# Optimization experiments

Measured on AMD Instinct MI355X. Metric: run time of the kernel, lower is better.

## Reference

```python
import jax, jax.numpy as jnp
import numpy as np

FILL_VAL = -1
B, S, H, L = 16, 512, 768, 25


def _lstm_dir(x, w_ih, w_hh, b_ih, b_hh, reverse=False):
    # x: [B,T,I]; PyTorch gate order i,f,g,o
    if reverse:
        x = x[:, ::-1]
    xg = jnp.einsum('bti,gi->btg', x, w_ih) + b_ih + b_hh  # [B,T,4H]
    nh = w_hh.shape[1]

    def step(carry, xt):
        h, c = carry
        g = xt + h @ w_hh.T
        i, f, gg, o = jnp.split(g, 4, axis=-1)
        c = jax.nn.sigmoid(f) * c + jax.nn.sigmoid(i) * jnp.tanh(gg)
        h = jax.nn.sigmoid(o) * jnp.tanh(c)
        return (h, c), h

    z = jnp.zeros((x.shape[0], nh), x.dtype)
    _, hs = jax.lax.scan(step, (z, z), jnp.swapaxes(xg, 0, 1))
    hs = jnp.swapaxes(hs, 0, 1)  # [B,T,H]
    return hs[:, ::-1] if reverse else hs


def _crf_nll(emissions, tags, mask, trans, start, end):
    # torchcrf-style NLL, reduction='token_mean'. emissions [B,T,L], tags [B,T], mask bool [B,T]
    maskf = mask.astype(emissions.dtype)
    emit = jnp.take_along_axis(emissions, tags[..., None], axis=-1)[..., 0]  # [B,T]
    trans_sc = trans[tags[:, :-1], tags[:, 1:]]  # [B,T-1]
    num = start[tags[:, 0]] + emit[:, 0] + jnp.sum((trans_sc + emit[:, 1:]) * maskf[:, 1:], axis=1)
    lengths = mask.sum(axis=1)
    last_tags = tags[jnp.arange(tags.shape[0]), lengths - 1]
    num = num + end[last_tags]

    em_t = jnp.swapaxes(emissions, 0, 1)  # [T,B,L]
    mk_t = jnp.swapaxes(mask, 0, 1)

    def step(alpha, inp):
        e_t, m_t = inp
        nxt = jax.nn.logsumexp(alpha[:, :, None] + trans[None] + e_t[:, None, :], axis=1)
        return jnp.where(m_t[:, None], nxt, alpha), None

    alpha0 = start[None] + em_t[0]
    alpha, _ = jax.lax.scan(step, alpha0, (em_t[1:], mk_t[1:]))
    denom = jax.nn.logsumexp(alpha + end[None], axis=1)
    llh = num - denom
    return -(llh.sum() / maskf.sum())


def setup_inputs() -> dict:
    key = jax.random.key(0)
    ks = jax.random.split(key, 32)

    def u(k, shape, s):
        return jax.random.uniform(k, shape, jnp.float32, -s, s)

    s = 1.0 / float(np.sqrt(H))
    hidden = jax.random.normal(ks[0], (B, S, H), jnp.float32)
    labels = jax.random.randint(ks[1], (B, S), 0, L)
    lengths = jax.random.randint(ks[2], (B,), S // 2, S + 1)
    targets = jnp.where(jnp.arange(S)[None, :] < lengths[:, None], labels, FILL_VAL).astype(jnp.int32)

    inp = {'hidden': hidden, 'targets': targets}
    # 2-layer bidirectional LSTM params; layer 1 input is 2H
    names = [('l0', H), ('l0r', H), ('l1', 2 * H), ('l1r', 2 * H)]
    ki = 3
    for nm, insz in names:
        inp['w_ih_' + nm] = u(ks[ki], (4 * H, insz), s); ki += 1
        inp['w_hh_' + nm] = u(ks[ki], (4 * H, H), s); ki += 1
        inp['b_ih_' + nm] = u(ks[ki], (4 * H,), s); ki += 1
        inp['b_hh_' + nm] = u(ks[ki], (4 * H,), s); ki += 1
    inp['clf_w'] = u(ks[ki], (L, 2 * H), 1.0 / float(np.sqrt(2 * H))); ki += 1
    inp['clf_b'] = u(ks[ki], (L,), 1.0 / float(np.sqrt(2 * H))); ki += 1
    inp['crf_trans'] = u(ks[ki], (L, L), 0.1); ki += 1
    inp['crf_start'] = u(ks[ki], (L,), 0.1); ki += 1
    inp['crf_end'] = u(ks[ki], (L,), 0.1)
    return inp


def reference(hidden, targets,
              w_ih_l0, w_hh_l0, b_ih_l0, b_hh_l0,
              w_ih_l0r, w_hh_l0r, b_ih_l0r, b_hh_l0r,
              w_ih_l1, w_hh_l1, b_ih_l1, b_hh_l1,
              w_ih_l1r, w_hh_l1r, b_ih_l1r, b_hh_l1r,
              clf_w, clf_b, crf_trans, crf_start, crf_end):
    mask = targets != FILL_VAL
    tags = jnp.where(mask, targets, 0)
    h1 = jnp.concatenate([
        _lstm_dir(hidden, w_ih_l0, w_hh_l0, b_ih_l0, b_hh_l0),
        _lstm_dir(hidden, w_ih_l0r, w_hh_l0r, b_ih_l0r, b_hh_l0r, reverse=True)], axis=-1)
    h2 = jnp.concatenate([
        _lstm_dir(h1, w_ih_l1, w_hh_l1, b_ih_l1, b_hh_l1),
        _lstm_dir(h1, w_ih_l1r, w_hh_l1r, b_ih_l1r, b_hh_l1r, reverse=True)], axis=-1)
    logits = jnp.tanh(h2) @ clf_w.T + clf_b  # [B,S,L]
    return _crf_nll(logits, tags, mask, crf_trans, crf_start, crf_end)
```

## Files before the change

kernel.cpp:

```cpp
#include <hip/hip_runtime.h>
#include <cstdint>
#include <cstddef>

#define B   16
#define SEQ 512
#define HD  768
#define G4  3072
#define NL  25
#define NBLK 96

using u16 = unsigned short;
using u32 = uint32_t;
using u64 = unsigned long long;

#define XGD ((size_t)96*SEQ*512)

__device__ __forceinline__ float bf2f(u16 u){
  union { float f; u32 i; } v; v.i = ((u32)u) << 16; return v.f;
}
__device__ __forceinline__ u16 f2bf(float f){
  union { float f; u32 i; } v; v.f = f;
  u32 r = v.i + 0x7FFFu + ((v.i >> 16) & 1u);
  return (u16)(r >> 16);
}
__device__ __forceinline__ float asf(u32 u){ union { float f; u32 i; } v; v.i = u; return v.f; }
__device__ __forceinline__ float sigm(float x){ return 1.f/(1.f + __expf(-x)); }
__device__ __forceinline__ float tanhfast(float x){ return 1.f - 2.f/(__expf(2.f*x) + 1.f); }

typedef __attribute__((ext_vector_type(8))) short bf16x8;
typedef __attribute__((ext_vector_type(4))) float f32x4;

__device__ __forceinline__ void stage_to_lds(u16* dst, const u16* src){
  *(uint4*)dst = *(const uint4*)src;
}
__device__ __forceinline__ void stage_to_lds(u16* dst, const float* src){
  float4 a = *(const float4*)src;
  float4 b = *(const float4*)(src + 4);
  uint4 v;
  v.x = (u32)f2bf(a.x) | ((u32)f2bf(a.y) << 16);
  v.y = (u32)f2bf(a.z) | ((u32)f2bf(a.w) << 16);
  v.z = (u32)f2bf(b.x) | ((u32)f2bf(b.y) << 16);
  v.w = (u32)f2bf(b.z) | ((u32)f2bf(b.w) << 16);
  *(uint4*)dst = v;
}

struct BPtrs { const float* bi[4]; const float* bh[4]; };

__global__ void prep_bias(BPtrs p, float* __restrict__ bias){
  int idx = blockIdx.x*blockDim.x + threadIdx.x;
  if (idx < 4*G4){
    int lid = idx / G4, g = idx % G4;
    bias[idx] = p.bi[lid][g] + p.bh[lid][g];
  }
}

template<typename AT>
__global__ __launch_bounds__(256) void gemm_xg_mfma(const AT* __restrict__ A, int K,
    const float* __restrict__ W, const float* __restrict__ bias, u16* __restrict__ out)
{
  __shared__ u16 As[128][72];
  __shared__ u16 Bs[128][72];
  const int tid = threadIdx.x;
  const int bm = blockIdx.y * 128;
  const int bn = blockIdx.x * 128;
  const int wid = tid >> 6, lane = tid & 63;
  const int wr = wid >> 1, wc = wid & 1;
  const int kq = lane >> 4, rl = lane & 15;

  f32x4 acc[4][4];
  #pragma unroll
  for (int mf = 0; mf < 4; mf++)
    #pragma unroll
    for (int nf = 0; nf < 4; nf++) acc[mf][nf] = (f32x4){0.f,0.f,0.f,0.f};

  for (int k0 = 0; k0 < K; k0 += 64){
    #pragma unroll
    for (int u = 0; u < 4; u++){
      int c = tid + u*256;
      int r = c >> 3, q = c & 7;
      stage_to_lds(&As[r][q*8], A + (size_t)(bm + r)*K + k0 + q*8);
      stage_to_lds(&Bs[r][q*8], W + (size_t)(bn + r)*K + k0 + q*8);
    }
    __syncthreads();
    #pragma unroll
    for (int sub = 0; sub < 2; sub++){
      bf16x8 af4[4], bfr4[4];
      #pragma unroll
      for (int mf = 0; mf < 4; mf++)
        af4[mf]  = *(const bf16x8*)&As[wr*64 + mf*16 + rl][sub*32 + kq*8];
      #pragma unroll
      for (int nf = 0; nf < 4; nf++)
        bfr4[nf] = *(const bf16x8*)&Bs[wc*64 + nf*16 + rl][sub*32 + kq*8];
      #pragma unroll
      for (int mf = 0; mf < 4; mf++)
        #pragma unroll
        for (int nf = 0; nf < 4; nf++)
          acc[mf][nf] = __builtin_amdgcn_mfma_f32_16x16x32_bf16(af4[mf], bfr4[nf], acc[mf][nf], 0, 0, 0);
    }
    __syncthreads();
  }

  float bv[4];
  size_t coloff[4];
  #pragma unroll
  for (int nf = 0; nf < 4; nf++){
    int n = bn + wc*64 + nf*16 + rl;
    bv[nf] = bias[n];
    int g = n / 768, j = n - g*768;
    coloff[nf] = (size_t)(j >> 3)*262144 + (size_t)g*128 + (j & 7);
  }
  #pragma unroll
  for (int mf = 0; mf < 4; mf++){
    #pragma unroll
    for (int i = 0; i < 4; i++){
      int row = bm + wr*64 + mf*16 + kq*4 + i;
      int b = row >> 9, t = row & 511;
      size_t rowoff = (size_t)t*512 + (size_t)b*8;
      #pragma unroll
      for (int nf = 0; nf < 4; nf++)
        out[coloff[nf] + rowoff] = f2bf(acc[mf][nf][i] + bv[nf]);
    }
  }
}

template<int LAYER>
__global__ __launch_bounds__(256, 1) void scan_kernel(
    const u16* __restrict__ xgp,
    const float* __restrict__ whh_f,
    const float* __restrict__ whh_r,
    u16* __restrict__ hgbu,
    u32* __restrict__ flags,
    u16* __restrict__ hout)
{
  __shared__ float red[32*16*4];
  __shared__ float cL[128];

  const int tid  = threadIdx.x;
  const int dir  = blockIdx.x / NBLK;
  const int js   = blockIdx.x % NBLK;
  const int w    = tid >> 6;
  const int lane = tid & 63;
  const int lr   = lane & 15;
  const int lq   = lane >> 4;

  const float* Wsrc = dir ? whh_r : whh_f;

  bf16x8 af[2][6];
  #pragma unroll
  for (int m = 0; m < 2; m++){
    int j_local = m*16 + lr;
    int j_glob  = (j_local >> 3)*768 + js*8 + (j_local & 7);
    const float* rowp = Wsrc + (size_t)j_glob*HD;
    #pragma unroll
    for (int c = 0; c < 6; c++){
      int k = w*192 + c*32 + lq*8;
      float4 a  = *(const float4*)(rowp + k);
      float4 b4 = *(const float4*)(rowp + k + 4);
      union { u32 u[4]; bf16x8 v; } t;
      t.u[0] = (u32)f2bf(a.x)  | ((u32)f2bf(a.y)  << 16);
      t.u[1] = (u32)f2bf(a.z)  | ((u32)f2bf(a.w)  << 16);
      t.u[2] = (u32)f2bf(b4.x) | ((u32)f2bf(b4.y) << 16);
      t.u[3] = (u32)f2bf(b4.z) | ((u32)f2bf(b4.w) << 16);
      af[m][c] = t.v;
    }
  }
  if (tid < 128) cL[tid] = 0.f;
  __syncthreads();

  const int jh_l = tid >> 4;
  const int b_g  = tid & 15;
  u32* myflag = flags + dir*NBLK;

  for (int s = 0; s < SEQ; s++){
    const int t_seq = dir ? (SEQ-1-s) : s;

    float xgv[4];
    if (tid < 128){
      const u16* xp = xgp + (size_t)dir*XGD + (size_t)js*262144
                    + (size_t)t_seq*512 + b_g*8 + jh_l;
      #pragma unroll
      for (int g = 0; g < 4; g++) xgv[g] = bf2f(xp[g*128]);
    }

    if (s > 0){
      if (tid < NBLK){
        while (__hip_atomic_load(&myflag[tid], __ATOMIC_RELAXED, __HIP_MEMORY_SCOPE_AGENT) < (u32)s)
          __builtin_amdgcn_s_sleep(1);
      }
      __syncthreads();
    }

    const u16* hb = hgbu + (size_t)((s&1)*2 + dir)*(16*768) + lr*768;
    u64 bq[6][2];
    #pragma unroll
    for (int c = 0; c < 6; c++){
      const u64* p = (const u64*)(hb + w*192 + c*32 + lq*8);
      bq[c][0] = __hip_atomic_load(p,     __ATOMIC_RELAXED, __HIP_MEMORY_SCOPE_AGENT);
      bq[c][1] = __hip_atomic_load(p + 1, __ATOMIC_RELAXED, __HIP_MEMORY_SCOPE_AGENT);
    }

    f32x4 acc0 = (f32x4){0.f,0.f,0.f,0.f};
    f32x4 acc1 = (f32x4){0.f,0.f,0.f,0.f};
    #pragma unroll
    for (int c = 0; c < 6; c++){
      union { u64 q[2]; bf16x8 v; } bu;
      bu.q[0] = bq[c][0]; bu.q[1] = bq[c][1];
      acc0 = __builtin_amdgcn_mfma_f32_16x16x32_bf16(af[0][c], bu.v, acc0, 0, 0, 0);
      acc1 = __builtin_amdgcn_mfma_f32_16x16x32_bf16(af[1][c], bu.v, acc1, 0, 0, 0);
    }

    #pragma unroll
    for (int i = 0; i < 4; i++){
      red[(( 0 + lq*4 + i)*16 + lr)*4 + w] = acc0[i];
      red[((16 + lq*4 + i)*16 + lr)*4 + w] = acc1[i];
    }
    __syncthreads();

    const bool more = (s + 1 < SEQ);
    u32 opair = 0;
    if (tid < 128){
      float gs[4];
      #pragma unroll
      for (int g = 0; g < 4; g++){
        const float4 r4 = *(const float4*)&red[((g*8 + jh_l)*16 + b_g)*4];
        gs[g] = r4.x + r4.y + r4.z + r4.w + xgv[g];
      }
      float c  = cL[tid];
      float ct = sigm(gs[1])*c + sigm(gs[0])*tanhfast(gs[2]);
      float h  = sigm(gs[3])*tanhfast(ct);
      cL[tid] = ct;

      u32 hb16 = (u32)f2bf(h);
      u32 hoth = (u32)__shfl_xor((int)hb16, 16);
      float hw = (LAYER == 0) ? h : tanhfast(h);
      u32 ob16 = (u32)f2bf(hw);
      u32 ooth = (u32)__shfl_xor((int)ob16, 16);
      opair = (ob16 & 0xffffu) | (ooth << 16);

      if (more && (tid & 16) == 0){
        u32 pair = (hb16 & 0xffffu) | (hoth << 16);
        u16* hdst = hgbu + (size_t)(((s+1)&1)*2 + dir)*(16*768) + b_g*768 + js*8 + jh_l;
        __hip_atomic_store((u32*)hdst, pair, __ATOMIC_RELAXED, __HIP_MEMORY_SCOPE_AGENT);
      }
    }
    if (more){
      __syncthreads();
      if (tid == 0)
        __hip_atomic_store(&myflag[js], (u32)(s+1), __ATOMIC_RELAXED, __HIP_MEMORY_SCOPE_AGENT);
    }
    if (tid < 128 && (tid & 16) == 0){
      u16* od = hout + ((size_t)b_g*SEQ + t_seq)*1536 + dir*HD + js*8 + jh_l;
      *(u32*)od = opair;
    }
  }
}

__global__ __launch_bounds__(256) void logits_kernel(const u16* __restrict__ th,
    const float* __restrict__ clf_w, const float* __restrict__ clf_b,
    float* __restrict__ logits)
{
  __shared__ u16 xl[8*1536];
  const int tid = threadIdx.x;
  const int row0 = blockIdx.x * 8;
  {
    const uint4* src = (const uint4*)(th + (size_t)row0*1536);
    uint4* dst = (uint4*)xl;
    #pragma unroll
    for (int i = 0; i < 6; i++) dst[i*256 + tid] = src[i*256 + tid];
  }
  __syncthreads();
  const int r = tid >> 5, l = tid & 31;
  if (l < NL){
    float acc = clf_b[l];
    const float* wr = clf_w + (size_t)l*1536;
    #pragma unroll 2
    for (int kk = 0; kk < 192; kk++){
      uint4 xv = *(const uint4*)&xl[r*1536 + kk*8];
      float4 w0 = *(const float4*)(wr + kk*8);
      float4 w1 = *(const float4*)(wr + kk*8 + 4);
      acc = fmaf(asf(xv.x<<16), w0.x, acc); acc = fmaf(asf(xv.x&0xffff0000u), w0.y, acc);
      acc = fmaf(asf(xv.y<<16), w0.z, acc); acc = fmaf(asf(xv.y&0xffff0000u), w0.w, acc);
      acc = fmaf(asf(xv.z<<16), w1.x, acc); acc = fmaf(asf(xv.z&0xffff0000u), w1.y, acc);
      acc = fmaf(asf(xv.w<<16), w1.z, acc); acc = fmaf(asf(xv.w&0xffff0000u), w1.w, acc);
    }
    logits[(size_t)(row0 + r)*NL + l] = acc;
  }
}

__global__ __launch_bounds__(256) void crf_num(const float* __restrict__ logits,
    const int* __restrict__ targets, const float* __restrict__ trans,
    const float* __restrict__ start, const float* __restrict__ endv,
    float* __restrict__ numlen)
{
  const int b = blockIdx.x;
  const int* tg = targets + (size_t)b*SEQ;
  float s = 0.f; int cnt = 0;
  for (int t = threadIdx.x; t < SEQ; t += 256){
    int cur = tg[t];
    if (cur >= 0){
      cnt++;
      float e = logits[((size_t)b*SEQ + t)*NL + cur];
      s += e;
      if (t > 0) s += trans[tg[t-1]*NL + cur];
    }
  }
  __shared__ float ss[256]; __shared__ int sc[256];
  ss[threadIdx.x] = s; sc[threadIdx.x] = cnt;
  __syncthreads();
  for (int o = 128; o > 0; o >>= 1){
    if (threadIdx.x < o){ ss[threadIdx.x] += ss[threadIdx.x+o]; sc[threadIdx.x] += sc[threadIdx.x+o]; }
    __syncthreads();
  }
  if (threadIdx.x == 0){
    int len = sc[0];
    numlen[b]      = ss[0] + start[tg[0]] + endv[tg[len-1]];
    numlen[16 + b] = (float)len;
  }
}

__global__ __launch_bounds__(64) void crf_fwd(const float* __restrict__ logits,
    const int* __restrict__ targets, const float* __restrict__ trans,
    const float* __restrict__ start, const float* __restrict__ endv,
    float* __restrict__ denom)
{
  const int b = blockIdx.x, lane = threadIdx.x;
  __shared__ float el[SEQ*NL];
  __shared__ float tr[NL*NL];
  for (int i = lane; i < NL*NL; i += 64) tr[i] = trans[i];
  {
    const float4* src = (const float4*)(logits + (size_t)b*SEQ*NL);
    float4* dst = (float4*)el;
    for (int i = lane; i < SEQ*NL/4; i += 64) dst[i] = src[i];
  }
  __syncthreads();
  const bool act = lane < NL;
  const int j = act ? lane : 0;
  float alpha = act ? (start[j] + el[j]) : -3e38f;
  const int* tg = targets + (size_t)b*SEQ;
  for (int t = 1; t < SEQ; t++){
    if (tg[t] < 0) break;
    float e = el[t*NL + j];
    float v[NL]; float mx = -3e38f;
    #pragma unroll
    for (int i = 0; i < NL; i++){
      float ai = __shfl(alpha, i);
      v[i] = ai + tr[i*NL + j];
      mx = fmaxf(mx, v[i]);
    }
    float sum = 0.f;
    #pragma unroll
    for (int i = 0; i < NL; i++) sum += __expf(v[i] - mx);
    float nxt = mx + __logf(sum) + e;
    if (act) alpha = nxt;
  }
  float x = act ? alpha + endv[j] : -3e38f;
  float m2 = x;
  #pragma unroll
  for (int off = 32; off >= 1; off >>= 1) m2 = fmaxf(m2, __shfl_xor(m2, off));
  float se = __expf(x - m2);
  #pragma unroll
  for (int off = 32; off >= 1; off >>= 1) se += __shfl_xor(se, off);
  if (lane == 0) denom[b] = m2 + __logf(se);
}

__global__ void crf_final(const float* __restrict__ numlen, const float* __restrict__ denom,
                          float* __restrict__ out)
{
  if (blockIdx.x == 0 && threadIdx.x == 0){
    float sn = 0.f, sl = 0.f;
    for (int b = 0; b < 16; b++){ sn += numlen[b] - denom[b]; sl += numlen[16+b]; }
    out[0] = -sn / sl;
  }
}

extern "C" void kernel_launch(void* const* d_in, const int* in_sizes, int n_in,
                              void* d_out, int out_size, void* d_ws, size_t ws_size,
                              hipStream_t stream)
{
  const float* hidden  = (const float*)d_in[0];
  const int*   targets = (const int*)  d_in[1];
  const float* w_ih[4] = {(const float*)d_in[2], (const float*)d_in[6], (const float*)d_in[10], (const float*)d_in[14]};
  const float* w_hh[4] = {(const float*)d_in[3], (const float*)d_in[7], (const float*)d_in[11], (const float*)d_in[15]};
  const float* b_ih[4] = {(const float*)d_in[4], (const float*)d_in[8], (const float*)d_in[12], (const float*)d_in[16]};
  const float* b_hh[4] = {(const float*)d_in[5], (const float*)d_in[9], (const float*)d_in[13], (const float*)d_in[17]};
  const float* clf_w = (const float*)d_in[18];
  const float* clf_b = (const float*)d_in[19];
  const float* trans = (const float*)d_in[20];
  const float* start = (const float*)d_in[21];
  const float* endv  = (const float*)d_in[22];

  char* p = (char*)d_ws;
  auto alloc = [&](size_t bytes){ void* r = (void*)p; p += (bytes + 255) & ~(size_t)255; return r; };
  float* bias   = (float*)alloc((size_t)4*G4*4);
  u16*   xgp    = (u16*)  alloc((size_t)2*XGD*2);
  u16*   h1     = (u16*)  alloc((size_t)B*SEQ*2*HD*2);
  u16*   hgbu   = (u16*)  alloc((size_t)2*2*16*768*2);
  u32*   flags  = (u32*)  alloc((size_t)2*NBLK*4);
  float* logits = (float*)alloc((size_t)B*SEQ*NL*4);
  float* numlen = (float*)alloc(32*4);
  float* denom  = (float*)alloc(16*4);
  if ((size_t)(p - (char*)d_ws) > ws_size) return;

  BPtrs bp;
  for (int i = 0; i < 4; i++){ bp.bi[i] = b_ih[i]; bp.bh[i] = b_hh[i]; }
  prep_bias<<<48, 256, 0, stream>>>(bp, bias);

  const dim3 ggrid(24, 64);
  const size_t hgb_bytes = (size_t)2*2*16*768*2;
  const size_t flg_bytes = (size_t)2*NBLK*4;

  gemm_xg_mfma<float><<<ggrid, 256, 0, stream>>>(hidden, HD, w_ih[0], bias + 0*G4, xgp);
  gemm_xg_mfma<float><<<ggrid, 256, 0, stream>>>(hidden, HD, w_ih[1], bias + 1*G4, xgp + XGD);
  hipMemsetAsync(hgbu, 0, hgb_bytes, stream);
  hipMemsetAsync(flags, 0, flg_bytes, stream);
  {
    const u16* a0 = xgp; const float* a1 = w_hh[0]; const float* a2 = w_hh[1];
    u16* a3 = hgbu; u32* a4 = flags; u16* a5 = h1;
    void* args[] = { &a0, &a1, &a2, &a3, &a4, &a5 };
    hipLaunchCooperativeKernel(reinterpret_cast<void*>(&scan_kernel<0>),
                               dim3(2*NBLK), dim3(256), args, 0, stream);
  }

  gemm_xg_mfma<u16><<<ggrid, 256, 0, stream>>>(h1, 2*HD, w_ih[2], bias + 2*G4, xgp);
  gemm_xg_mfma<u16><<<ggrid, 256, 0, stream>>>(h1, 2*HD, w_ih[3], bias + 3*G4, xgp + XGD);
  hipMemsetAsync(hgbu, 0, hgb_bytes, stream);
  hipMemsetAsync(flags, 0, flg_bytes, stream);
  {
    const u16* a0 = xgp; const float* a1 = w_hh[2]; const float* a2 = w_hh[3];
    u16* a3 = hgbu; u32* a4 = flags; u16* a5 = h1;
    void* args[] = { &a0, &a1, &a2, &a3, &a4, &a5 };
    hipLaunchCooperativeKernel(reinterpret_cast<void*>(&scan_kernel<1>),
                               dim3(2*NBLK), dim3(256), args, 0, stream);
  }

  logits_kernel<<<1024, 256, 0, stream>>>(h1, clf_w, clf_b, logits);
  crf_num<<<16, 256, 0, stream>>>(logits, targets, trans, start, endv, numlen);
  crf_fwd<<<16, 64, 0, stream>>>(logits, targets, trans, start, endv, denom);
  crf_final<<<1, 64, 0, stream>>>(numlen, denom, (float*)d_out);
}
```

Baseline: 4.083 ms.

## Pre-convert input weights to bf16 and stage GEMM tiles via direct global-to-LDS loads

```diff
diff --git a/kernel.cpp b/kernel.cpp
--- a/kernel.cpp
+++ b/kernel.cpp
@@ -30,9 +30,12 @@
 typedef __attribute__((ext_vector_type(8))) short bf16x8;
 typedef __attribute__((ext_vector_type(4))) float f32x4;
 
-__device__ __forceinline__ void stage_to_lds(u16* dst, const u16* src){
-  *(uint4*)dst = *(const uint4*)src;
-}
+__device__ __forceinline__ void gload16(const u16* g, u16* l){
+  __builtin_amdgcn_global_load_lds(
+      (const __attribute__((address_space(1))) void*)g,
+      (__attribute__((address_space(3))) void*)l, 16, 0, 0);
+}
+
 __device__ __forceinline__ void stage_to_lds(u16* dst, const float* src){
   float4 a = *(const float4*)src;
   float4 b = *(const float4*)(src + 4);
@@ -54,12 +57,40 @@
   }
 }
 
+__global__ void conv_bf16(const float* __restrict__ src, u16* __restrict__ dst, int n8){
+  for (int i = blockIdx.x*blockDim.x + threadIdx.x; i < n8; i += gridDim.x*blockDim.x)
+    stage_to_lds(dst + (size_t)i*8, src + (size_t)i*8);
+}
+
+__device__ __forceinline__ void stage_tile(u16* Ls, const u16* A, size_t ldk,
+                                           int base_row, int k0, int wid, int lane){
+  #pragma unroll
+  for (int i = 0; i < 4; i++){
+    int cbase = i*256 + wid*64;
+    int c  = cbase + lane;
+    int rs = c >> 3, qs = c & 7;
+    int qg = qs ^ (rs & 7);
+    gload16(A + (size_t)(base_row + rs)*ldk + k0 + qg*8, Ls + (size_t)cbase*8);
+  }
+}
+__device__ __forceinline__ void stage_tile(u16* Ls, const float* A, size_t ldk,
+                                           int base_row, int k0, int wid, int lane){
+  const int tid = wid*64 + lane;
+  #pragma unroll
+  for (int i = 0; i < 4; i++){
+    int c  = i*256 + tid;
+    int rs = c >> 3, qs = c & 7;
+    int qg = qs ^ (rs & 7);
+    stage_to_lds(Ls + rs*64 + qs*8, A + (size_t)(base_row + rs)*ldk + k0 + qg*8);
+  }
+}
+
 template<typename AT>
 __global__ __launch_bounds__(256) void gemm_xg_mfma(const AT* __restrict__ A, int K,
-    const float* __restrict__ W, const float* __restrict__ bias, u16* __restrict__ out)
-{
-  __shared__ u16 As[128][72];
-  __shared__ u16 Bs[128][72];
+    const u16* __restrict__ W, const float* __restrict__ bias, u16* __restrict__ out)
+{
+  __shared__ u16 As[128*64];
+  __shared__ u16 Bs[128*64];
   const int tid = threadIdx.x;
   const int bm = blockIdx.y * 128;
   const int bn = blockIdx.x * 128;
@@ -74,23 +105,22 @@
     for (int nf = 0; nf < 4; nf++) acc[mf][nf] = (f32x4){0.f,0.f,0.f,0.f};
 
   for (int k0 = 0; k0 < K; k0 += 64){
-    #pragma unroll
-    for (int u = 0; u < 4; u++){
-      int c = tid + u*256;
-      int r = c >> 3, q = c & 7;
-      stage_to_lds(&As[r][q*8], A + (size_t)(bm + r)*K + k0 + q*8);
-      stage_to_lds(&Bs[r][q*8], W + (size_t)(bn + r)*K + k0 + q*8);
-    }
+    stage_tile(Bs, W, (size_t)K, bn, k0, wid, lane);
+    stage_tile(As, A, (size_t)K, bm, k0, wid, lane);
     __syncthreads();
     #pragma unroll
     for (int sub = 0; sub < 2; sub++){
       bf16x8 af4[4], bfr4[4];
       #pragma unroll
-      for (int mf = 0; mf < 4; mf++)
-        af4[mf]  = *(const bf16x8*)&As[wr*64 + mf*16 + rl][sub*32 + kq*8];
-      #pragma unroll
-      for (int nf = 0; nf < 4; nf++)
-        bfr4[nf] = *(const bf16x8*)&Bs[wc*64 + nf*16 + rl][sub*32 + kq*8];
+      for (int mf = 0; mf < 4; mf++){
+        int r = wr*64 + mf*16 + rl;
+        af4[mf]  = *(const bf16x8*)&As[r*64 + (((sub<<2)|kq) ^ (r & 7))*8];
+      }
+      #pragma unroll
+      for (int nf = 0; nf < 4; nf++){
+        int r = wc*64 + nf*16 + rl;
+        bfr4[nf] = *(const bf16x8*)&Bs[r*64 + (((sub<<2)|kq) ^ (r & 7))*8];
+      }
       #pragma unroll
       for (int mf = 0; mf < 4; mf++)
         #pragma unroll
@@ -399,6 +429,7 @@
   float* logits = (float*)alloc((size_t)B*SEQ*NL*4);
   float* numlen = (float*)alloc(32*4);
   float* denom  = (float*)alloc(16*4);
+  u16*   wb     = (u16*)  alloc((size_t)2*3072*1536*2);
   if ((size_t)(p - (char*)d_ws) > ws_size) return;
 
   BPtrs bp;
@@ -408,9 +439,13 @@
   const dim3 ggrid(24, 64);
   const size_t hgb_bytes = (size_t)2*2*16*768*2;
   const size_t flg_bytes = (size_t)2*NBLK*4;
-
-  gemm_xg_mfma<float><<<ggrid, 256, 0, stream>>>(hidden, HD, w_ih[0], bias + 0*G4, xgp);
-  gemm_xg_mfma<float><<<ggrid, 256, 0, stream>>>(hidden, HD, w_ih[1], bias + 1*G4, xgp + XGD);
+  const size_t w0 = (size_t)3072*768;
+  const size_t w1 = (size_t)3072*1536;
+
+  conv_bf16<<<512, 256, 0, stream>>>(w_ih[0], wb,      (int)(w0/8));
+  conv_bf16<<<512, 256, 0, stream>>>(w_ih[1], wb + w0, (int)(w0/8));
+  gemm_xg_mfma<float><<<ggrid, 256, 0, stream>>>(hidden, HD, wb,      bias + 0*G4, xgp);
+  gemm_xg_mfma<float><<<ggrid, 256, 0, stream>>>(hidden, HD, wb + w0, bias + 1*G4, xgp + XGD);
   hipMemsetAsync(hgbu, 0, hgb_bytes, stream);
   hipMemsetAsync(flags, 0, flg_bytes, stream);
   {
@@ -421,8 +456,10 @@
                                dim3(2*NBLK), dim3(256), args, 0, stream);
   }
 
-  gemm_xg_mfma<u16><<<ggrid, 256, 0, stream>>>(h1, 2*HD, w_ih[2], bias + 2*G4, xgp);
-  gemm_xg_mfma<u16><<<ggrid, 256, 0, stream>>>(h1, 2*HD, w_ih[3], bias + 3*G4, xgp + XGD);
+  conv_bf16<<<512, 256, 0, stream>>>(w_ih[2], wb,      (int)(w1/8));
+  conv_bf16<<<512, 256, 0, stream>>>(w_ih[3], wb + w1, (int)(w1/8));
+  gemm_xg_mfma<u16><<<ggrid, 256, 0, stream>>>(h1, 2*HD, wb,      bias + 2*G4, xgp);
+  gemm_xg_mfma<u16><<<ggrid, 256, 0, stream>>>(h1, 2*HD, wb + w1, bias + 3*G4, xgp + XGD);
   hipMemsetAsync(hgbu, 0, hgb_bytes, stream);
   hipMemsetAsync(flags, 0, flg_bytes, stream);
   {
```

After: 3.980 ms. 1.03x faster.
